# Optimization experiments

Measured on AMD Instinct MI355X. Metric: run time of the kernel, lower is better.

## Reference

```python
import jax, jax.numpy as jnp
import numpy as np

DIM = 256
NUM_LAYERS = 6
STRENGTHS = jnp.array([0.1, 0.1, 0.05], dtype=jnp.float32)  # entail, contra, neutral
MAX_NORM = 10.0
EPS = 1e-8          # ops.eps()
NORM_EPS = 1e-12    # F.normalize eps
B = 131072


def _normalize(x, axis=-1):
    # matches torch F.normalize(p=2): x / max(||x||, 1e-12)
    n = jnp.linalg.norm(x, axis=axis, keepdims=True)
    return x / jnp.maximum(n, NORM_EPS)


def setup_inputs() -> dict:
    key = jax.random.key(0)
    ks = jax.random.split(key, 6)
    return {
        "h0": jax.random.normal(ks[0], (B, DIM), dtype=jnp.float32),
        "W1": jax.random.normal(ks[1], (DIM, DIM), dtype=jnp.float32) * 0.05,
        "b1": jax.random.normal(ks[2], (DIM,), dtype=jnp.float32) * 0.05,
        "W2": jax.random.normal(ks[3], (DIM, DIM), dtype=jnp.float32) * 0.05,
        "b2": jax.random.normal(ks[4], (DIM,), dtype=jnp.float32) * 0.05,
        "anchors": jax.random.normal(ks[5], (3, DIM), dtype=jnp.float32),
    }


def reference(h0, W1, b1, W2, b2, anchors):
    anchors_n = _normalize(anchors, axis=-1)  # [3, D], normalized once before the loop

    def step(h, _):
        h_n = _normalize(h)                              # [B, D]
        # physics: alignment = cos sim, divergence = 1 - alignment, tension = div^2
        align = h_n @ anchors_n.T                        # [B, 3]
        div = 1.0 - align                                # [B, 3]
        tens = div * div                                 # [B, 3] (traced, not fed back)
        # anchor forces: -strength * div * normalize(h - anchor)
        direction = _normalize(h[:, None, :] - anchors_n[None, :, :])   # [B, 3, D]
        total_force = jnp.einsum('bk,bkd->bd', -(STRENGTHS[None, :] * div), direction)
        # 2-layer MLP update
        delta = jnp.tanh(h @ W1.T + b1) @ W2.T + b2      # [B, D]
        h_new = h + delta + total_force
        # norm clipping
        n = jnp.linalg.norm(h_new, axis=-1, keepdims=True)
        h_new = jnp.where(n > MAX_NORM, h_new * (MAX_NORM / (n + EPS)), h_new)
        return h_new, (align, div, tens)

    h_final, (aligns, divs, tens) = jax.lax.scan(step, h0, None, length=NUM_LAYERS)
    # aligns/divs/tens: [L, B, 3] traces, axis -1 = (entail, contra, neutral)
    return h_final, aligns, divs, tens
```

## Files before the change

kernel.cpp:

```cpp
#include <hip/hip_runtime.h>
#include <math.h>


#define DIMX 256
#define NL 6
#define CPAD 68

typedef float f32x4 __attribute__((ext_vector_type(4)));
typedef short short8 __attribute__((ext_vector_type(8)));
typedef unsigned int u32x4 __attribute__((ext_vector_type(4)));

#define CHB(c) ((c) * 1024)
#define EXTB 16384
#define STATB 17408

#define PACKB(X0, X1, DST)                                                       \
    asm("v_cvt_pk_bf16_f32 %0, %1, %2" : "=v"(DST) : "v"(X0), "v"(X1));

__global__ void wsplit(const float* __restrict__ W1, const float* __restrict__ W2,
                       const float* __restrict__ anchors, const float* __restrict__ b2f,
                       u32x4* __restrict__ ws) {
    int gi = blockIdx.x * 256 + threadIdx.x;
    if (gi < 16384) {
        int ln   = gi & 63;
        int t8   = (gi >> 6) & 7;
        int ks2  = (gi >> 9) & 1;
        int kk   = (gi >> 10) & 3;
        int pass = (gi >> 12) & 1;
        int g    = (gi >> 13) & 1;
        int ks   = kk * 2 + ks2;
        int m    = (pass * 8 + t8) * 16 + (ln & 15);
        int G    = ln >> 4;
        const float* Wg = g ? W2 : W1;
        unsigned o[4];
#pragma unroll
        for (int p = 0; p < 4; ++p) {
            int f = 32 * ks + ((p >> 1) << 4) + 4 * G + ((p & 1) << 1);
            float x0 = Wg[m * DIMX + f];
            float x1 = Wg[m * DIMX + f + 1];
            unsigned hp;
            PACKB(x0, x1, hp);
            o[p] = hp;
        }
        u32x4 out = {o[0], o[1], o[2], o[3]};
        ws[gi] = out;
    } else if (gi < STATB) {
        int r    = gi - EXTB;
        int pass = r >> 9;
        int t8   = (r >> 6) & 7;
        int ln   = r & 63;
        int m    = ln & 15;
        int G    = ln >> 4;
        int fout = (pass * 8 + t8) * 16 + m;
        float inv[3];
#pragma unroll
        for (int k = 0; k < 3; ++k) {
            float ss = 0.0f;
            for (int f = 0; f < DIMX; ++f) { float a = anchors[k*DIMX+f]; ss += a*a; }
            inv[k] = 1.0f / fmaxf(sqrtf(ss), 1e-12f);
        }
        float v[8];
#pragma unroll
        for (int i = 0; i < 8; ++i) {
            int k = G * 8 + i;
            v[i] = (k == 0) ? -anchors[fout] * inv[0]
                 : (k == 1) ? -anchors[DIMX + fout] * inv[1]
                 : (k == 2) ? -anchors[2 * DIMX + fout] * inv[2]
                 : (k == 3) ? b2f[fout] : 0.0f;
        }
        unsigned o[4];
#pragma unroll
        for (int p = 0; p < 4; ++p) { unsigned hp; PACKB(v[2*p], v[2*p+1], hp); o[p] = hp; }
        u32x4 out = {o[0], o[1], o[2], o[3]};
        ws[gi] = out;
    } else if (gi < STATB + 512) {
        int r  = gi - STATB;
        int ks = r >> 6;
        int ln = r & 63;
        int m  = ln & 15;
        int G  = ln >> 4;
        float inv = 0.0f;
        if (m < 3) {
            float ss = 0.0f;
            for (int f = 0; f < DIMX; ++f) { float a = anchors[m*DIMX+f]; ss += a*a; }
            inv = 1.0f / fmaxf(sqrtf(ss), 1e-12f);
        }
        float v[8];
#pragma unroll
        for (int i = 0; i < 8; ++i) {
            int f = 32 * ks + 16 * (i >> 2) + 4 * G + (i & 3);
            v[i] = (m < 3) ? anchors[m * DIMX + f] * inv : 0.0f;
        }
        unsigned o[4];
#pragma unroll
        for (int p = 0; p < 4; ++p) { unsigned hp; PACKB(v[2*p], v[2*p+1], hp); o[p] = hp; }
        u32x4 out = {o[0], o[1], o[2], o[3]};
        ws[gi] = out;
    }
}


#define STAGE(gIdxBase, ldsSlotBase)                                             \
    {                                                                            \
        _Pragma("unroll")                                                        \
        for (int i_ = 0; i_ < 2; ++i_) {                                         \
            const int off_ = ((w * 2 + i_) << 6);                                \
            __builtin_amdgcn_global_load_lds(                                    \
                (const __attribute__((address_space(1))) void*)(ws + (gIdxBase) + off_ + lane), \
                (__attribute__((address_space(3))) void*)(&wf[(ldsSlotBase) + off_]),           \
                16, 0, 0);                                                       \
        }                                                                        \
    }

#define PIPE_SYNC()                                                              \
    {                                                                            \
        asm volatile("s_waitcnt vmcnt(4)" ::: "memory");                         \
        __builtin_amdgcn_sched_barrier(0);                                       \
        __builtin_amdgcn_s_barrier();                                            \
        __builtin_amdgcn_sched_barrier(0);                                       \
    }

__global__ __launch_bounds__(512, 2)
void collapse_mfma16(const float* __restrict__ h0,
                     const float* __restrict__ b1f,
                     const u32x4* __restrict__ ws,
                     float* __restrict__ out_h,
                     float* __restrict__ out_align,
                     float* __restrict__ out_div,
                     float* __restrict__ out_tens,
                     int B)
{
    __shared__ __align__(16) u32x4 wf[4096];
    __shared__ __align__(16) u32x4 wext[1024];
    __shared__ __align__(16) u32x4 wstat[512];
    __shared__ __align__(16) float b1_reg[272];

    const int tid  = threadIdx.x;
    const int w    = tid >> 6;
    const int lane = tid & 63;
    const int G    = lane >> 4;
    const int c    = lane & 15;
    const int bglob = blockIdx.x * 128 + w * 16 + c;

    {
#pragma unroll
        for (int i_ = 0; i_ < 2; ++i_) {
            const int off_ = ((w * 2 + i_) << 6);
            __builtin_amdgcn_global_load_lds(
                (const __attribute__((address_space(1))) void*)(ws + EXTB + off_ + lane),
                (__attribute__((address_space(3))) void*)(&wext[off_]),
                16, 0, 0);
        }
        __builtin_amdgcn_global_load_lds(
            (const __attribute__((address_space(1))) void*)(ws + STATB + w*64 + lane),
            (__attribute__((address_space(3))) void*)(&wstat[w*64]),
            16, 0, 0);
    }

    {
        int idx = tid & 255;
        int Gc = idx >> 6, s = idx & 63;
        int f = 16 * (s >> 2) + 4 * Gc + (s & 3);
        if (tid < 256) b1_reg[Gc * CPAD + s] = b1f[f];
    }
    __syncthreads();

    float hr[64];
#pragma unroll
    for (int mt = 0; mt < 16; ++mt) {
        const float4 v = *(const float4*)&h0[(size_t)bglob * DIMX + 16 * mt + 4 * G];
        hr[mt * 4 + 0] = v.x; hr[mt * 4 + 1] = v.y;
        hr[mt * 4 + 2] = v.z; hr[mt * 4 + 3] = v.w;
    }

    STAGE(CHB(0), 0);
    STAGE(CHB(1), 1024);
    STAGE(CHB(2), 2048);

#pragma unroll 1
    for (int layer = 0; layer < NL; ++layer) {
        float p0 = 0;
#pragma unroll
        for (int s = 0; s < 64; ++s) p0 += hr[s] * hr[s];
        p0 += __shfl_xor(p0, 16);
        p0 += __shfl_xor(p0, 32);

        unsigned tph[32];
        f32x4 acs = (f32x4)(0.0f);
#pragma unroll
        for (int pass = 0; pass < 2; ++pass) {
            f32x4 ac[8];
#pragma unroll
            for (int j = 0; j < 8; ++j) ac[j] = (f32x4)(0.0f);
#pragma unroll
            for (int kk = 0; kk < 4; ++kk) {
                const int s = pass * 4 + kk;
                PIPE_SYNC();
                STAGE(CHB((s + 3) & 15), ((s + 3) & 3) * 1024);
                const int cb = (s & 3) * 1024;
#pragma unroll
                for (int ks2 = 0; ks2 < 2; ++ks2) {
                    const int ks = kk * 2 + ks2;
                    unsigned bh[4];
#pragma unroll
                    for (int p = 0; p < 4; ++p)
                        PACKB(hr[8*ks + 2*p], hr[8*ks + 2*p + 1], bh[p]);
                    u32x4 thi = {bh[0], bh[1], bh[2], bh[3]};
                    const short8 Bh = __builtin_bit_cast(short8, thi);
#pragma unroll
                    for (int j = 0; j < 8; ++j) {
                        const short8 Ah = __builtin_bit_cast(short8,
                            wf[cb + ks2*512 + j*64 + lane]);
                        ac[j] = __builtin_amdgcn_mfma_f32_16x16x32_bf16(Ah, Bh, ac[j], 0, 0, 0);
                    }
                    if (pass == 0) {
                        const short8 As = __builtin_bit_cast(short8, wstat[ks*64 + lane]);
                        acs = __builtin_amdgcn_mfma_f32_16x16x32_bf16(As, Bh, acs, 0, 0, 0);
                    }
                }
            }
#pragma unroll
            for (int j = 0; j < 8; ++j) {
                const int mt = pass * 8 + j;
                const float4 bq = *(const float4*)&b1_reg[G * CPAD + mt * 4];
                float tv[4];
#pragma unroll
                for (int r = 0; r < 4; ++r) {
                    float x = ac[j][r] + ((r==0)?bq.x:(r==1)?bq.y:(r==2)?bq.z:bq.w);
                    float e = __expf(2.0f * x);
                    tv[r] = 1.0f - 2.0f * __builtin_amdgcn_rcpf(e + 1.0f);
                }
                const int ti = 4 * (mt >> 1) + 2 * (mt & 1);
                PACKB(tv[0], tv[1], tph[ti]);
                PACKB(tv[2], tv[3], tph[ti + 1]);
            }
        }

        const float d0 = acs[0], d1 = acs[1], d2 = acs[2];
        const float inv_rn = 1.0f / fmaxf(sqrtf(p0), 1e-12f);
        const float al0 = d0 * inv_rn, al1 = d1 * inv_rn, al2 = d2 * inv_rn;
        const float dv0 = 1.0f - al0, dv1 = 1.0f - al1, dv2 = 1.0f - al2;
        const float c0 = -0.10f * dv0 / fmaxf(sqrtf(fmaxf(p0 - 2.0f*d0 + 1.0f, 0.0f)), 1e-12f);
        const float c1 = -0.10f * dv1 / fmaxf(sqrtf(fmaxf(p0 - 2.0f*d1 + 1.0f, 0.0f)), 1e-12f);
        const float c2 = -0.05f * dv2 / fmaxf(sqrtf(fmaxf(p0 - 2.0f*d2 + 1.0f, 0.0f)), 1e-12f);
        if (G == 0) {
            const long long tb = ((long long)layer * B + bglob) * 3;
            out_align[tb+0] = al0; out_align[tb+1] = al1; out_align[tb+2] = al2;
            out_div[tb+0] = dv0;   out_div[tb+1] = dv1;   out_div[tb+2] = dv2;
            out_tens[tb+0] = dv0*dv0; out_tens[tb+1] = dv1*dv1; out_tens[tb+2] = dv2*dv2;
        }
        unsigned be0 = 0, be1 = 0;
        if (G == 0) { PACKB(c0, c1, be0); PACKB(c2, 1.0f, be1); }
        u32x4 bev = {be0, be1, 0u, 0u};
        const short8 Bext = __builtin_bit_cast(short8, bev);
        float csum = 1.0f + c0 + c1 + c2;
        csum = __shfl(csum, c);

#pragma unroll
        for (int pass = 0; pass < 2; ++pass) {
            f32x4 ac[8];
#pragma unroll
            for (int j = 0; j < 8; ++j) {
                const int mt = pass * 8 + j;
                ac[j][0] = hr[mt*4+0]*csum;
                ac[j][1] = hr[mt*4+1]*csum;
                ac[j][2] = hr[mt*4+2]*csum;
                ac[j][3] = hr[mt*4+3]*csum;
            }
#pragma unroll
            for (int j = 0; j < 8; ++j) {
                const short8 Ax = __builtin_bit_cast(short8, wext[pass*512 + j*64 + lane]);
                ac[j] = __builtin_amdgcn_mfma_f32_16x16x32_bf16(Ax, Bext, ac[j], 0, 0, 0);
            }
#pragma unroll
            for (int kk = 0; kk < 4; ++kk) {
                const int s = 8 + pass * 4 + kk;
                PIPE_SYNC();
                STAGE(CHB((s + 3) & 15), ((s + 3) & 3) * 1024);
                const int cb = (s & 3) * 1024;
#pragma unroll
                for (int ks2 = 0; ks2 < 2; ++ks2) {
                    const int ks = kk * 2 + ks2;
                    u32x4 thi = {tph[4*ks+0], tph[4*ks+1], tph[4*ks+2], tph[4*ks+3]};
                    const short8 Bh = __builtin_bit_cast(short8, thi);
#pragma unroll
                    for (int j = 0; j < 8; ++j) {
                        const short8 Ah = __builtin_bit_cast(short8,
                            wf[cb + ks2*512 + j*64 + lane]);
                        ac[j] = __builtin_amdgcn_mfma_f32_16x16x32_bf16(Ah, Bh, ac[j], 0, 0, 0);
                    }
                }
            }
#pragma unroll
            for (int j = 0; j < 8; ++j) {
                const int mt = pass * 8 + j;
                hr[mt*4+0] = ac[j][0]; hr[mt*4+1] = ac[j][1];
                hr[mt*4+2] = ac[j][2]; hr[mt*4+3] = ac[j][3];
            }
        }

        {
            float ss = 0.0f;
#pragma unroll
            for (int s = 0; s < 64; ++s) ss += hr[s] * hr[s];
            ss += __shfl_xor(ss, 16);
            ss += __shfl_xor(ss, 32);
            const float n = sqrtf(ss);
            const float sc = (n > 10.0f) ? (10.0f / (n + 1e-8f)) : 1.0f;
#pragma unroll
            for (int s = 0; s < 64; ++s) hr[s] *= sc;
        }
    }

#pragma unroll
    for (int mt = 0; mt < 16; ++mt) {
        float4 v;
        v.x = hr[mt*4+0]; v.y = hr[mt*4+1]; v.z = hr[mt*4+2]; v.w = hr[mt*4+3];
        *(float4*)&out_h[(size_t)bglob * DIMX + 16 * mt + 4 * G] = v;
    }
}

extern "C" void kernel_launch(void* const* d_in, const int* in_sizes, int n_in,
                              void* d_out, int out_size, void* d_ws, size_t ws_size,
                              hipStream_t stream) {
    const float* h0      = (const float*)d_in[0];
    const float* W1      = (const float*)d_in[1];
    const float* b1      = (const float*)d_in[2];
    const float* W2      = (const float*)d_in[3];
    const float* b2      = (const float*)d_in[4];
    const float* anchors = (const float*)d_in[5];
    const int B = in_sizes[0] / DIMX;

    float* out_h     = (float*)d_out;
    float* out_align = out_h + (long long)B * DIMX;
    float* out_div   = out_align + (long long)NL * B * 3;
    float* out_tens  = out_div   + (long long)NL * B * 3;

    u32x4* ws = (u32x4*)d_ws;

    hipLaunchKernelGGL(wsplit, dim3(70), dim3(256), 0, stream, W1, W2, anchors, b2, ws);
    hipLaunchKernelGGL(collapse_mfma16, dim3(B / 128), dim3(512), 0, stream,
                       h0, b1, ws,
                       out_h, out_align, out_div, out_tens, B);
}
```

Measured before the change: 337.0 us.

## Process two 16-row batch tiles per wave to reuse staged weight fragments

Each wave now holds two 16-row batch tiles of h in registers, so every weight fragment read from LDS feeds two MFMAs instead of one. This halves the number of blocks and the total weight-staging traffic per row. The cost is a doubled register footprint: launch bounds drop from 2 to 1 blocks per CU, which cuts occupancy and latency hiding and may cause register spills.

After: 558.8 us. +65.8%, slower.

```diff
diff --git a/kernel.cpp b/kernel.cpp
--- a/kernel.cpp
+++ b/kernel.cpp
@@ -120,7 +120,7 @@
         __builtin_amdgcn_sched_barrier(0);                                       \
     }
 
-__global__ __launch_bounds__(512, 2)
+__global__ __launch_bounds__(512, 1)
 void collapse_mfma16(const float* __restrict__ h0,
                      const float* __restrict__ b1f,
                      const u32x4* __restrict__ ws,
@@ -140,7 +140,7 @@
     const int lane = tid & 63;
     const int G    = lane >> 4;
     const int c    = lane & 15;
-    const int bglob = blockIdx.x * 128 + w * 16 + c;
+    const int bg   = blockIdx.x * 256 + w * 32 + c;
 
     {
 #pragma unroll
@@ -165,12 +165,16 @@
     }
     __syncthreads();
 
-    float hr[64];
-#pragma unroll
-    for (int mt = 0; mt < 16; ++mt) {
-        const float4 v = *(const float4*)&h0[(size_t)bglob * DIMX + 16 * mt + 4 * G];
-        hr[mt * 4 + 0] = v.x; hr[mt * 4 + 1] = v.y;
-        hr[mt * 4 + 2] = v.z; hr[mt * 4 + 3] = v.w;
+    float hr[2][64];
+#pragma unroll
+    for (int bt = 0; bt < 2; ++bt) {
+#pragma unroll
+        for (int mt = 0; mt < 16; ++mt) {
+            const float4 v = *(const float4*)
+                &h0[(size_t)(bg + bt*16) * DIMX + 16 * mt + 4 * G];
+            hr[bt][mt*4+0] = v.x; hr[bt][mt*4+1] = v.y;
+            hr[bt][mt*4+2] = v.z; hr[bt][mt*4+3] = v.w;
+        }
     }
 
     STAGE(CHB(0), 0);
@@ -179,19 +183,27 @@
 
 #pragma unroll 1
     for (int layer = 0; layer < NL; ++layer) {
-        float p0 = 0;
-#pragma unroll
-        for (int s = 0; s < 64; ++s) p0 += hr[s] * hr[s];
-        p0 += __shfl_xor(p0, 16);
-        p0 += __shfl_xor(p0, 32);
-
-        unsigned tph[32];
-        f32x4 acs = (f32x4)(0.0f);
+        float p0[2];
+#pragma unroll
+        for (int bt = 0; bt < 2; ++bt) {
+            float s_ = 0.0f;
+#pragma unroll
+            for (int s = 0; s < 64; ++s) s_ += hr[bt][s] * hr[bt][s];
+            s_ += __shfl_xor(s_, 16);
+            s_ += __shfl_xor(s_, 32);
+            p0[bt] = s_;
+        }
+
+        unsigned tph[2][32];
+        f32x4 acs[2];
+        acs[0] = (f32x4)(0.0f); acs[1] = (f32x4)(0.0f);
 #pragma unroll
         for (int pass = 0; pass < 2; ++pass) {
-            f32x4 ac[8];
-#pragma unroll
-            for (int j = 0; j < 8; ++j) ac[j] = (f32x4)(0.0f);
+            f32x4 ac[2][8];
+#pragma unroll
+            for (int bt = 0; bt < 2; ++bt)
+#pragma unroll
+                for (int j = 0; j < 8; ++j) ac[bt][j] = (f32x4)(0.0f);
 #pragma unroll
             for (int kk = 0; kk < 4; ++kk) {
                 const int s = pass * 4 + kk;
@@ -201,21 +213,28 @@
 #pragma unroll
                 for (int ks2 = 0; ks2 < 2; ++ks2) {
                     const int ks = kk * 2 + ks2;
-                    unsigned bh[4];
-#pragma unroll
-                    for (int p = 0; p < 4; ++p)
-                        PACKB(hr[8*ks + 2*p], hr[8*ks + 2*p + 1], bh[p]);
-                    u32x4 thi = {bh[0], bh[1], bh[2], bh[3]};
-                    const short8 Bh = __builtin_bit_cast(short8, thi);
+                    short8 Bh[2];
+#pragma unroll
+                    for (int bt = 0; bt < 2; ++bt) {
+                        unsigned b0_, b1_, b2_, b3_;
+                        PACKB(hr[bt][8*ks+0], hr[bt][8*ks+1], b0_);
+                        PACKB(hr[bt][8*ks+2], hr[bt][8*ks+3], b1_);
+                        PACKB(hr[bt][8*ks+4], hr[bt][8*ks+5], b2_);
+                        PACKB(hr[bt][8*ks+6], hr[bt][8*ks+7], b3_);
+                        u32x4 bv = {b0_, b1_, b2_, b3_};
+                        Bh[bt] = __builtin_bit_cast(short8, bv);
+                    }
 #pragma unroll
                     for (int j = 0; j < 8; ++j) {
                         const short8 Ah = __builtin_bit_cast(short8,
                             wf[cb + ks2*512 + j*64 + lane]);
-                        ac[j] = __builtin_amdgcn_mfma_f32_16x16x32_bf16(Ah, Bh, ac[j], 0, 0, 0);
+                        ac[0][j] = __builtin_amdgcn_mfma_f32_16x16x32_bf16(Ah, Bh[0], ac[0][j], 0, 0, 0);
+                        ac[1][j] = __builtin_amdgcn_mfma_f32_16x16x32_bf16(Ah, Bh[1], ac[1][j], 0, 0, 0);
                     }
                     if (pass == 0) {
                         const short8 As = __builtin_bit_cast(short8, wstat[ks*64 + lane]);
-                        acs = __builtin_amdgcn_mfma_f32_16x16x32_bf16(As, Bh, acs, 0, 0, 0);
+                        acs[0] = __builtin_amdgcn_mfma_f32_16x16x32_bf16(As, Bh[0], acs[0], 0, 0, 0);
+                        acs[1] = __builtin_amdgcn_mfma_f32_16x16x32_bf16(As, Bh[1], acs[1], 0, 0, 0);
                     }
                 }
             }
@@ -223,54 +242,70 @@
             for (int j = 0; j < 8; ++j) {
                 const int mt = pass * 8 + j;
                 const float4 bq = *(const float4*)&b1_reg[G * CPAD + mt * 4];
-                float tv[4];
-#pragma unroll
-                for (int r = 0; r < 4; ++r) {
-                    float x = ac[j][r] + ((r==0)?bq.x:(r==1)?bq.y:(r==2)?bq.z:bq.w);
-                    float e = __expf(2.0f * x);
-                    tv[r] = 1.0f - 2.0f * __builtin_amdgcn_rcpf(e + 1.0f);
-                }
                 const int ti = 4 * (mt >> 1) + 2 * (mt & 1);
-                PACKB(tv[0], tv[1], tph[ti]);
-                PACKB(tv[2], tv[3], tph[ti + 1]);
-            }
-        }
-
-        const float d0 = acs[0], d1 = acs[1], d2 = acs[2];
-        const float inv_rn = 1.0f / fmaxf(sqrtf(p0), 1e-12f);
-        const float al0 = d0 * inv_rn, al1 = d1 * inv_rn, al2 = d2 * inv_rn;
-        const float dv0 = 1.0f - al0, dv1 = 1.0f - al1, dv2 = 1.0f - al2;
-        const float c0 = -0.10f * dv0 / fmaxf(sqrtf(fmaxf(p0 - 2.0f*d0 + 1.0f, 0.0f)), 1e-12f);
-        const float c1 = -0.10f * dv1 / fmaxf(sqrtf(fmaxf(p0 - 2.0f*d1 + 1.0f, 0.0f)), 1e-12f);
-        const float c2 = -0.05f * dv2 / fmaxf(sqrtf(fmaxf(p0 - 2.0f*d2 + 1.0f, 0.0f)), 1e-12f);
-        if (G == 0) {
-            const long long tb = ((long long)layer * B + bglob) * 3;
-            out_align[tb+0] = al0; out_align[tb+1] = al1; out_align[tb+2] = al2;
-            out_div[tb+0] = dv0;   out_div[tb+1] = dv1;   out_div[tb+2] = dv2;
-            out_tens[tb+0] = dv0*dv0; out_tens[tb+1] = dv1*dv1; out_tens[tb+2] = dv2*dv2;
-        }
-        unsigned be0 = 0, be1 = 0;
-        if (G == 0) { PACKB(c0, c1, be0); PACKB(c2, 1.0f, be1); }
-        u32x4 bev = {be0, be1, 0u, 0u};
-        const short8 Bext = __builtin_bit_cast(short8, bev);
-        float csum = 1.0f + c0 + c1 + c2;
-        csum = __shfl(csum, c);
-
+#pragma unroll
+                for (int bt = 0; bt < 2; ++bt) {
+                    float tv[4];
+#pragma unroll
+                    for (int r = 0; r < 4; ++r) {
+                        float x = ac[bt][j][r] + ((r==0)?bq.x:(r==1)?bq.y:(r==2)?bq.z:bq.w);
+                        float e = __expf(2.0f * x);
+                        tv[r] = 1.0f - 2.0f * __builtin_amdgcn_rcpf(e + 1.0f);
+                    }
+                    PACKB(tv[0], tv[1], tph[bt][ti]);
+                    PACKB(tv[2], tv[3], tph[bt][ti + 1]);
+                }
+            }
+        }
+
+        float csum[2];
+        unsigned be0[2] = {0u, 0u}, be1[2] = {0u, 0u};
+#pragma unroll
+        for (int bt = 0; bt < 2; ++bt) {
+            const float d0 = acs[bt][0], d1 = acs[bt][1], d2 = acs[bt][2];
+            const float inv_rn = 1.0f / fmaxf(sqrtf(p0[bt]), 1e-12f);
+            const float al0 = d0*inv_rn, al1 = d1*inv_rn, al2 = d2*inv_rn;
+            const float dv0 = 1.0f-al0, dv1 = 1.0f-al1, dv2 = 1.0f-al2;
+            const float c0 = -0.10f*dv0 / fmaxf(sqrtf(fmaxf(p0[bt]-2.0f*d0+1.0f, 0.0f)), 1e-12f);
+            const float c1 = -0.10f*dv1 / fmaxf(sqrtf(fmaxf(p0[bt]-2.0f*d1+1.0f, 0.0f)), 1e-12f);
+            const float c2 = -0.05f*dv2 / fmaxf(sqrtf(fmaxf(p0[bt]-2.0f*d2+1.0f, 0.0f)), 1e-12f);
+            if (G == 0) {
+                const long long tb = ((long long)layer * B + (bg + bt*16)) * 3;
+                out_align[tb+0] = al0; out_align[tb+1] = al1; out_align[tb+2] = al2;
+                out_div[tb+0] = dv0;   out_div[tb+1] = dv1;   out_div[tb+2] = dv2;
+                out_tens[tb+0] = dv0*dv0; out_tens[tb+1] = dv1*dv1; out_tens[tb+2] = dv2*dv2;
+                PACKB(c0, c1, be0[bt]);
+                PACKB(c2, 1.0f, be1[bt]);
+            }
+            float cs = 1.0f + c0 + c1 + c2;
+            csum[bt] = __shfl(cs, c);
+        }
+
+        short8 Bext[2];
+#pragma unroll
+        for (int bt = 0; bt < 2; ++bt) {
+            u32x4 bev = {be0[bt], be1[bt], 0u, 0u};
+            Bext[bt] = __builtin_bit_cast(short8, bev);
+        }
 #pragma unroll
         for (int pass = 0; pass < 2; ++pass) {
-            f32x4 ac[8];
+            f32x4 ac[2][8];
 #pragma unroll
             for (int j = 0; j < 8; ++j) {
                 const int mt = pass * 8 + j;
-                ac[j][0] = hr[mt*4+0]*csum;
-                ac[j][1] = hr[mt*4+1]*csum;
-                ac[j][2] = hr[mt*4+2]*csum;
-                ac[j][3] = hr[mt*4+3]*csum;
+#pragma unroll
+                for (int bt = 0; bt < 2; ++bt) {
+                    ac[bt][j][0] = hr[bt][mt*4+0]*csum[bt];
+                    ac[bt][j][1] = hr[bt][mt*4+1]*csum[bt];
+                    ac[bt][j][2] = hr[bt][mt*4+2]*csum[bt];
+                    ac[bt][j][3] = hr[bt][mt*4+3]*csum[bt];
+                }
             }
 #pragma unroll
             for (int j = 0; j < 8; ++j) {
                 const short8 Ax = __builtin_bit_cast(short8, wext[pass*512 + j*64 + lane]);
-                ac[j] = __builtin_amdgcn_mfma_f32_16x16x32_bf16(Ax, Bext, ac[j], 0, 0, 0);
+                ac[0][j] = __builtin_amdgcn_mfma_f32_16x16x32_bf16(Ax, Bext[0], ac[0][j], 0, 0, 0);
+                ac[1][j] = __builtin_amdgcn_mfma_f32_16x16x32_bf16(Ax, Bext[1], ac[1][j], 0, 0, 0);
             }
 #pragma unroll
             for (int kk = 0; kk < 4; ++kk) {
@@ -281,42 +316,56 @@
 #pragma unroll
                 for (int ks2 = 0; ks2 < 2; ++ks2) {
                     const int ks = kk * 2 + ks2;
-                    u32x4 thi = {tph[4*ks+0], tph[4*ks+1], tph[4*ks+2], tph[4*ks+3]};
-                    const short8 Bh = __builtin_bit_cast(short8, thi);
+                    short8 Bh[2];
+#pragma unroll
+                    for (int bt = 0; bt < 2; ++bt) {
+                        u32x4 bv = {tph[bt][4*ks+0], tph[bt][4*ks+1],
+                                    tph[bt][4*ks+2], tph[bt][4*ks+3]};
+                        Bh[bt] = __builtin_bit_cast(short8, bv);
+                    }
 #pragma unroll
                     for (int j = 0; j < 8; ++j) {
                         const short8 Ah = __builtin_bit_cast(short8,
                             wf[cb + ks2*512 + j*64 + lane]);
-                        ac[j] = __builtin_amdgcn_mfma_f32_16x16x32_bf16(Ah, Bh, ac[j], 0, 0, 0);
+                        ac[0][j] = __builtin_amdgcn_mfma_f32_16x16x32_bf16(Ah, Bh[0], ac[0][j], 0, 0, 0);
+                        ac[1][j] = __builtin_amdgcn_mfma_f32_16x16x32_bf16(Ah, Bh[1], ac[1][j], 0, 0, 0);
                     }
                 }
             }
 #pragma unroll
             for (int j = 0; j < 8; ++j) {
                 const int mt = pass * 8 + j;
-                hr[mt*4+0] = ac[j][0]; hr[mt*4+1] = ac[j][1];
-                hr[mt*4+2] = ac[j][2]; hr[mt*4+3] = ac[j][3];
-            }
-        }
-
-        {
+#pragma unroll
+                for (int bt = 0; bt < 2; ++bt) {
+                    hr[bt][mt*4+0] = ac[bt][j][0]; hr[bt][mt*4+1] = ac[bt][j][1];
+                    hr[bt][mt*4+2] = ac[bt][j][2]; hr[bt][mt*4+3] = ac[bt][j][3];
+                }
+            }
+        }
+
+#pragma unroll
+        for (int bt = 0; bt < 2; ++bt) {
             float ss = 0.0f;
 #pragma unroll
-            for (int s = 0; s < 64; ++s) ss += hr[s] * hr[s];
+            for (int s = 0; s < 64; ++s) ss += hr[bt][s] * hr[bt][s];
             ss += __shfl_xor(ss, 16);
             ss += __shfl_xor(ss, 32);
             const float n = sqrtf(ss);
             const float sc = (n > 10.0f) ? (10.0f / (n + 1e-8f)) : 1.0f;
 #pragma unroll
-            for (int s = 0; s < 64; ++s) hr[s] *= sc;
-        }
-    }
-
-#pragma unroll
-    for (int mt = 0; mt < 16; ++mt) {
-        float4 v;
-        v.x = hr[mt*4+0]; v.y = hr[mt*4+1]; v.z = hr[mt*4+2]; v.w = hr[mt*4+3];
-        *(float4*)&out_h[(size_t)bglob * DIMX + 16 * mt + 4 * G] = v;
+            for (int s = 0; s < 64; ++s) hr[bt][s] *= sc;
+        }
+    }
+
+#pragma unroll
+    for (int bt = 0; bt < 2; ++bt) {
+#pragma unroll
+        for (int mt = 0; mt < 16; ++mt) {
+            float4 v;
+            v.x = hr[bt][mt*4+0]; v.y = hr[bt][mt*4+1];
+            v.z = hr[bt][mt*4+2]; v.w = hr[bt][mt*4+3];
+            *(float4*)&out_h[(size_t)(bg + bt*16) * DIMX + 16 * mt + 4 * G] = v;
+        }
     }
 }
 
@@ -339,7 +388,7 @@
     u32x4* ws = (u32x4*)d_ws;
 
     hipLaunchKernelGGL(wsplit, dim3(70), dim3(256), 0, stream, W1, W2, anchors, b2, ws);
-    hipLaunchKernelGGL(collapse_mfma16, dim3(B / 128), dim3(512), 0, stream,
+    hipLaunchKernelGGL(collapse_mfma16, dim3(B / 256), dim3(512), 0, stream,
                        h0, b1, ws,
                        out_h, out_align, out_div, out_tens, B);
 }
```

## Keep six weight chunks resident in LDS and double-buffer the rest

Applied to the files above, without the earlier changes.

Six of the sixteen bf16 weight chunks are now loaded into LDS once at kernel start and stay resident. The other ten are streamed through a two-slot double buffer, using a full vmcnt(0) wait and a barrier per window. This cuts per-layer global/L2 weight traffic and removes barriers for the resident chunks. In exchange the streamed chunks get a shallower prefetch depth than the old four-slot ring, and LDS use grows to about 153KB, which rules out a second block per CU.

Measured after the change: 327.8 us. -2.7%, faster.

```diff
diff --git a/kernel.cpp b/kernel.cpp
--- a/kernel.cpp
+++ b/kernel.cpp
@@ -100,24 +100,25 @@
 }
 
 
-#define STAGE(gIdxBase, ldsSlotBase)                                             \
+#define STAGE_TO(gIdxBase, ARR, ldsSlotBase)                                     \
     {                                                                            \
         _Pragma("unroll")                                                        \
         for (int i_ = 0; i_ < 2; ++i_) {                                         \
             const int off_ = ((w * 2 + i_) << 6);                                \
             __builtin_amdgcn_global_load_lds(                                    \
                 (const __attribute__((address_space(1))) void*)(ws + (gIdxBase) + off_ + lane), \
-                (__attribute__((address_space(3))) void*)(&wf[(ldsSlotBase) + off_]),           \
+                (__attribute__((address_space(3))) void*)(&ARR[(ldsSlotBase) + off_]),          \
                 16, 0, 0);                                                       \
         }                                                                        \
     }
 
-#define PIPE_SYNC()                                                              \
+#define WINDOW(pos)                                                              \
     {                                                                            \
-        asm volatile("s_waitcnt vmcnt(4)" ::: "memory");                         \
+        asm volatile("s_waitcnt vmcnt(0)" ::: "memory");                         \
         __builtin_amdgcn_sched_barrier(0);                                       \
         __builtin_amdgcn_s_barrier();                                            \
         __builtin_amdgcn_sched_barrier(0);                                       \
+        STAGE_TO(CHB(6 + (((pos) + 1) % 10)), wfs, ((((pos) + 1) & 1)) * 1024);  \
     }
 
 __global__ __launch_bounds__(512, 2)
@@ -130,7 +131,8 @@
                      float* __restrict__ out_tens,
                      int B)
 {
-    __shared__ __align__(16) u32x4 wf[4096];
+    __shared__ __align__(16) u32x4 wfr[6144];
+    __shared__ __align__(16) u32x4 wfs[2048];
     __shared__ __align__(16) u32x4 wext[1024];
     __shared__ __align__(16) u32x4 wstat[512];
     __shared__ __align__(16) float b1_reg[272];
@@ -155,6 +157,9 @@
             (const __attribute__((address_space(1))) void*)(ws + STATB + w*64 + lane),
             (__attribute__((address_space(3))) void*)(&wstat[w*64]),
             16, 0, 0);
+#pragma unroll
+        for (int cch = 0; cch < 6; ++cch) STAGE_TO(CHB(cch), wfr, cch * 1024);
+        STAGE_TO(CHB(6), wfs, 0);
     }
 
     {
@@ -173,10 +178,6 @@
         hr[mt * 4 + 2] = v.z; hr[mt * 4 + 3] = v.w;
     }
 
-    STAGE(CHB(0), 0);
-    STAGE(CHB(1), 1024);
-    STAGE(CHB(2), 2048);
-
 #pragma unroll 1
     for (int layer = 0; layer < NL; ++layer) {
         float p0 = 0;
@@ -195,9 +196,10 @@
 #pragma unroll
             for (int kk = 0; kk < 4; ++kk) {
                 const int s = pass * 4 + kk;
-                PIPE_SYNC();
-                STAGE(CHB((s + 3) & 15), ((s + 3) & 3) * 1024);
-                const int cb = (s & 3) * 1024;
+                const bool streamed = (s >= 6);
+                if (pass == 1 && kk == 2) WINDOW(0);
+                if (pass == 1 && kk == 3) WINDOW(1);
+                const int cb = streamed ? ((s - 6) & 1) * 1024 : s * 1024;
 #pragma unroll
                 for (int ks2 = 0; ks2 < 2; ++ks2) {
                     const int ks = kk * 2 + ks2;
@@ -209,8 +211,9 @@
                     const short8 Bh = __builtin_bit_cast(short8, thi);
 #pragma unroll
                     for (int j = 0; j < 8; ++j) {
-                        const short8 Ah = __builtin_bit_cast(short8,
-                            wf[cb + ks2*512 + j*64 + lane]);
+                        const short8 Ah = streamed
+                            ? __builtin_bit_cast(short8, wfs[cb + ks2*512 + j*64 + lane])
+                            : __builtin_bit_cast(short8, wfr[cb + ks2*512 + j*64 + lane]);
                         ac[j] = __builtin_amdgcn_mfma_f32_16x16x32_bf16(Ah, Bh, ac[j], 0, 0, 0);
                     }
                     if (pass == 0) {
@@ -274,10 +277,12 @@
             }
 #pragma unroll
             for (int kk = 0; kk < 4; ++kk) {
-                const int s = 8 + pass * 4 + kk;
-                PIPE_SYNC();
-                STAGE(CHB((s + 3) & 15), ((s + 3) & 3) * 1024);
-                const int cb = (s & 3) * 1024;
+                const int pos = 2 + pass * 4 + kk;
+                if (pos == 2) WINDOW(2); if (pos == 3) WINDOW(3);
+                if (pos == 4) WINDOW(4); if (pos == 5) WINDOW(5);
+                if (pos == 6) WINDOW(6); if (pos == 7) WINDOW(7);
+                if (pos == 8) WINDOW(8); if (pos == 9) WINDOW(9);
+                const int cb = (pos & 1) * 1024;
 #pragma unroll
                 for (int ks2 = 0; ks2 < 2; ++ks2) {
                     const int ks = kk * 2 + ks2;
@@ -286,7 +291,7 @@
 #pragma unroll
                     for (int j = 0; j < 8; ++j) {
                         const short8 Ah = __builtin_bit_cast(short8,
-                            wf[cb + ks2*512 + j*64 + lane]);
+                            wfs[cb + ks2*512 + j*64 + lane]);
                         ac[j] = __builtin_amdgcn_mfma_f32_16x16x32_bf16(Ah, Bh, ac[j], 0, 0, 0);
                     }
                 }
```
